# Kernel optimization log

Measured on AMD Instinct MI355X. Metric: run time of the kernel, lower is better.

## Reference

```python
import jax, jax.numpy as jnp
import numpy as np
import math

S, B, D, H = 2048, 4, 1024, 16
DH = D // H

def setup_inputs() -> dict:
    key = jax.random.key(0)
    ks = jax.random.split(key, 6)
    x = jax.random.normal(ks[0], (S, B, D), dtype=jnp.float32)
    # causal additive mask (finite large negative for numerical safety)
    i = jnp.arange(S)
    attn_mask = jnp.where(i[None, :] > i[:, None], jnp.float32(-1e9), jnp.float32(0.0))
    beta = jnp.zeros((H,), dtype=jnp.float32)  # per-head log-scale, init 0 -> exp=1
    xav = math.sqrt(6.0 / (D + D))  # xavier_uniform bound
    Wq = jax.random.uniform(ks[1], (D, D), minval=-xav, maxval=xav, dtype=jnp.float32)
    Wk = jax.random.uniform(ks[2], (D, D), minval=-xav, maxval=xav, dtype=jnp.float32)
    Wv = jax.random.uniform(ks[3], (D, D), minval=-xav, maxval=xav, dtype=jnp.float32)
    Wo = jax.random.uniform(ks[4], (D, D), minval=-xav, maxval=xav, dtype=jnp.float32)
    z = jnp.zeros((D,), dtype=jnp.float32)
    return {"x": x, "attn_mask": attn_mask, "beta": beta,
            "Wq": Wq, "bq": z, "Wk": Wk, "bk": z, "Wv": Wv, "bv": z, "Wo": Wo, "bo": z}

def reference(x, attn_mask, beta, Wq, bq, Wk, bk, Wv, bv, Wo, bo):
    s, b, d = x.shape
    h, dh = H, DH
    q = x @ Wq.T + bq  # (s, b, d)
    k = x @ Wk.T + bk
    v = x @ Wv.T + bv
    # attn_sink: append zero key/value token, pad mask with a zero column
    k = jnp.concatenate([k, jnp.zeros((1, b, d), k.dtype)], axis=0)  # (s+1, b, d)
    v = jnp.concatenate([v, jnp.zeros((1, b, d), v.dtype)], axis=0)
    mask = jnp.pad(attn_mask, ((0, 0), (0, 1)))  # (s, s+1)
    t = s + 1
    # split heads: (seq, b, h, dh) -> (b, h, seq, dh)
    qh = q.reshape(s, b, h, dh).transpose(1, 2, 0, 3)
    kh = k.reshape(t, b, h, dh).transpose(1, 2, 0, 3)
    vh = v.reshape(t, b, h, dh).transpose(1, 2, 0, 3)
    scale = (jnp.exp(beta) * math.sqrt(dh))[None, :, None, None]
    qh = qh / scale
    scores = jnp.einsum('bhsd,bhtd->bhst', qh, kh) + mask[None, None]
    w = jax.nn.softmax(scores, axis=-1)
    out = jnp.einsum('bhst,bhtd->bhsd', w, vh)  # (b, h, s, dh)
    out = out.transpose(2, 0, 1, 3).reshape(s, b, d)
    return out @ Wo.T + bo
```

## Files before the change

kernel.cpp:

```cpp
#include <hip/hip_runtime.h>
#include <hip/hip_bf16.h>
#include <math.h>

#define S_LEN   2048
#define BATCH   4
#define DMODEL  1024
#define NHEAD   16
#define DHEAD   64
#define MROWS   (S_LEN * BATCH)

typedef __bf16 bf16;
typedef __bf16 bf16x8 __attribute__((ext_vector_type(8)));
typedef __bf16 bf16x4 __attribute__((ext_vector_type(4)));
typedef short  short4_t __attribute__((ext_vector_type(4)));
typedef float  f32x4  __attribute__((ext_vector_type(4)));

#define LOG2E 1.4426950408889634f

#define AS1C(p) (const __attribute__((address_space(1))) void*)(p)
#define AS3(p)  (__attribute__((address_space(3))) void*)(p)


__global__ __launch_bounds__(256) void cast_bf16(const float* __restrict__ in,
                                                 bf16* __restrict__ out, int n8) {
    int i = blockIdx.x * 256 + threadIdx.x;
    if (i >= n8) return;
    const float4* p = (const float4*)in;
    float4 a = p[i * 2], b = p[i * 2 + 1];
    bf16x8 o;
    o[0] = (bf16)a.x; o[1] = (bf16)a.y; o[2] = (bf16)a.z; o[3] = (bf16)a.w;
    o[4] = (bf16)b.x; o[5] = (bf16)b.y; o[6] = (bf16)b.z; o[7] = (bf16)b.w;
    *(bf16x8*)(out + (size_t)i * 8) = o;
}

__global__ __launch_bounds__(256) void cast3_bf16(const float* __restrict__ w0,
                                                  const float* __restrict__ w1,
                                                  const float* __restrict__ w2,
                                                  bf16* __restrict__ out) {
    const int seg = blockIdx.y;
    const float* in = (seg == 0) ? w0 : (seg == 1) ? w1 : w2;
    int i = blockIdx.x * 256 + threadIdx.x;
    const float4* p = (const float4*)in;
    float4 a = p[i * 2], b = p[i * 2 + 1];
    bf16x8 o;
    o[0] = (bf16)a.x; o[1] = (bf16)a.y; o[2] = (bf16)a.z; o[3] = (bf16)a.w;
    o[4] = (bf16)b.x; o[5] = (bf16)b.y; o[6] = (bf16)b.z; o[7] = (bf16)b.w;
    *(bf16x8*)(out + (size_t)seg * DMODEL * DMODEL + (size_t)i * 8) = o;
}

#define GEMM_CORE(A_, W_, KDIM_)                                                        \
    constexpr int BK = 32;                                                              \
    __shared__ __align__(16) bf16 sA[128 * BK];                                         \
    __shared__ __align__(16) bf16 sB[128 * BK];                                         \
    const int t    = threadIdx.x;                                                       \
    const int lane = t & 63;                                                            \
    const int wave = t >> 6;                                                            \
    const int bm = blockIdx.y * 128;                                                    \
    const int wm = (wave & 1) * 64;                                                     \
    const int wn = (wave >> 1) * 64;                                                    \
    const int lq = lane & 15;                                                           \
    const int lg = lane >> 4;                                                           \
    const int grow = wave * 32 + (lane >> 2);                                           \
    const int gcol = (lane & 3) * 8;                                                    \
    const bf16* Ap = A_ + (size_t)(bm + grow) * KDIM_ + gcol;                           \
    const bf16* Wp = W_ + (size_t)(bn + grow) * KDIM_ + gcol;                           \
    bf16* la0 = &sA[(wave * 32) * BK];                                                  \
    bf16* lb0 = &sB[(wave * 32) * BK];                                                  \
    f32x4 acc[4][4] = {};                                                               \
    for (int k0 = 0; k0 < KDIM_; k0 += BK) {                                            \
        __syncthreads();                                                                \
        __builtin_amdgcn_global_load_lds(AS1C(Ap + k0),                      AS3(la0),           16, 0, 0); \
        __builtin_amdgcn_global_load_lds(AS1C(Ap + (size_t)16 * KDIM_ + k0), AS3(la0 + 16 * BK), 16, 0, 0); \
        __builtin_amdgcn_global_load_lds(AS1C(Wp + k0),                      AS3(lb0),           16, 0, 0); \
        __builtin_amdgcn_global_load_lds(AS1C(Wp + (size_t)16 * KDIM_ + k0), AS3(lb0 + 16 * BK), 16, 0, 0); \
        __syncthreads();                                                                \
        const int koff = lg * 8;                                                        \
        bf16x8 af[4], bfr[4];                                                           \
        _Pragma("unroll")                                                               \
        for (int mt = 0; mt < 4; mt++)                                                  \
            af[mt] = *(const bf16x8*)&sA[(wm + mt * 16 + lq) * BK + koff];              \
        _Pragma("unroll")                                                               \
        for (int nt = 0; nt < 4; nt++)                                                  \
            bfr[nt] = *(const bf16x8*)&sB[(wn + nt * 16 + lq) * BK + koff];             \
        _Pragma("unroll")                                                               \
        for (int mt = 0; mt < 4; mt++)                                                  \
            _Pragma("unroll")                                                           \
            for (int nt = 0; nt < 4; nt++)                                              \
                acc[mt][nt] = __builtin_amdgcn_mfma_f32_16x16x32_bf16(                  \
                    af[mt], bfr[nt], acc[mt][nt], 0, 0, 0);                             \
    }                                                                                   \
    const int cr = lg * 4;                                                              \
    const int cc = lq;

__global__ __launch_bounds__(256) void qkv_gemm(const bf16* __restrict__ A,
                                                const bf16* __restrict__ W,
                                                const float* __restrict__ bq,
                                                const float* __restrict__ bk,
                                                const float* __restrict__ bv,
                                                const float* __restrict__ beta,
                                                bf16* __restrict__ Qo,
                                                bf16* __restrict__ Kp,
                                                bf16* __restrict__ Vp) {
    const int bn = blockIdx.x * 128;
    GEMM_CORE(A, W, DMODEL)

    const int seg = blockIdx.x >> 3;
    const int bnl = (blockIdx.x & 7) * 128;
    const float* bias = (seg == 0) ? bq : (seg == 1) ? bk : bv;

    if (seg == 0) {
#pragma unroll
        for (int nt = 0; nt < 4; nt++) {
            const int col = bnl + wn + nt * 16 + cc;
            const float bvv = bias[col];
            const float sc = LOG2E / (__expf(beta[col >> 6]) * 8.0f);
#pragma unroll
            for (int mt = 0; mt < 4; mt++) {
                const int row = bm + wm + mt * 16 + cr;
#pragma unroll
                for (int r = 0; r < 4; r++) {
                    float v = (acc[mt][nt][r] + bvv) * sc;
                    Qo[(size_t)(row + r) * DMODEL + col] = (bf16)v;
                }
            }
        }
    } else {
        bf16* out = (seg == 1) ? Kp : Vp;
        const int h = (bnl + wn) >> 6;
#pragma unroll
        for (int mt = 0; mt < 4; mt++) {
            const int S0  = (bm + wm + mt * 16) >> 2;
            const int t16 = S0 >> 4;
            const int m4  = (S0 >> 2) & 3;
#pragma unroll
            for (int nt = 0; nt < 4; nt++) {
                const int col = bnl + wn + nt * 16 + cc;
                const float bvv = bias[col];
#pragma unroll
                for (int r = 0; r < 4; r++) {
                    float v = acc[mt][nt][r] + bvv;
                    size_t addr;
                    if (seg == 1) {
                        addr = ((size_t)((r * 16 + h) * 128 + t16)) * 1024
                             + (nt >> 1) * 512
                             + ((S0 & 15) + lg + 16 * ((nt & 1) * 2 + (lq >> 3))) * 8
                             + (lq & 7);
                    } else {
                        addr = ((size_t)((r * 16 + h) * 128 + t16)) * 1024
                             + nt * 256 + (lq + 16 * m4) * 4 + lg;
                    }
                    out[addr] = (bf16)v;
                }
            }
        }
    }
}

__global__ __launch_bounds__(256) void gemm_out(const bf16* __restrict__ A,
                                                const bf16* __restrict__ W,
                                                const float* __restrict__ bias,
                                                float* __restrict__ C) {
    const int bn = blockIdx.x * 128;
    GEMM_CORE(A, W, DMODEL)
#pragma unroll
    for (int nt = 0; nt < 4; nt++) {
        const int col = bn + wn + nt * 16 + cc;
        const float bvv = bias[col];
#pragma unroll
        for (int mt = 0; mt < 4; mt++) {
            const int row = bm + wm + mt * 16 + cr;
#pragma unroll
            for (int r = 0; r < 4; r++)
                C[(size_t)(row + r) * DMODEL + col] = acc[mt][nt][r] + bvv;
        }
    }
}

__global__ __launch_bounds__(256, 3) void attn_kernel(const bf16* __restrict__ Q,
                                                      const bf16* __restrict__ Kp,
                                                      const bf16* __restrict__ Vp,
                                                      bf16* __restrict__ O) {
    __shared__ __align__(16) float sO[64 * 65];
    __shared__ __align__(16) float sL[256];

    const int t    = threadIdx.x;
    const int lane = t & 63;
    const int wave = t >> 6;
    const int lq = lane & 15;
    const int lg = lane >> 4;

    const int bid = (int)blockIdx.x + 32 * ((int)blockIdx.y + 16 * (int)blockIdx.z);
    const int swz = (bid & 7) * 256 + (bid >> 3);
    const int qi  = 31 - (swz & 31);
    const int h   = (swz >> 5) & 15;
    const int b   = swz >> 9;
    const int qb  = qi * 64;

    bf16x8 qf[4][2];
#pragma unroll
    for (int nt = 0; nt < 4; nt++)
#pragma unroll
        for (int kc = 0; kc < 2; kc++)
            qf[nt][kc] = *(const bf16x8*)
                &Q[((size_t)(qb + nt * 16 + lq) * BATCH + b) * DMODEL + h * DHEAD + kc * 32 + lg * 8];

    f32x4 o_acc[4][4] = {};
    float l_lane[4] = {0.f, 0.f, 0.f, 0.f};

    const bf16* Kb = Kp + (size_t)(b * NHEAD + h) * 131072;
    const bf16* Vb = Vp + (size_t)(b * NHEAD + h) * 131072;

    bf16x8 kc0 = *(const bf16x8*)(Kb + (size_t)wave * 1024 + lane * 8);
    bf16x8 kc1 = *(const bf16x8*)(Kb + (size_t)wave * 1024 + 512 + lane * 8);
    bf16x4 vc0 = *(const bf16x4*)(Vb + (size_t)wave * 1024 +   0 + lane * 4);
    bf16x4 vc1 = *(const bf16x4*)(Vb + (size_t)wave * 1024 + 256 + lane * 4);
    bf16x4 vc2 = *(const bf16x4*)(Vb + (size_t)wave * 1024 + 512 + lane * 4);
    bf16x4 vc3 = *(const bf16x4*)(Vb + (size_t)wave * 1024 + 768 + lane * 4);

    for (int kt = 0; kt <= qi; kt++) {
        const int tn = ((kt < qi) ? (kt + 1) : 0) * 4 + wave;
        const bf16* Kn = Kb + (size_t)tn * 1024;
        const bf16* Vn = Vb + (size_t)tn * 1024;
        bf16x8 kn0 = *(const bf16x8*)(Kn + lane * 8);
        bf16x8 kn1 = *(const bf16x8*)(Kn + 512 + lane * 8);
        bf16x4 vn0 = *(const bf16x4*)(Vn +   0 + lane * 4);
        bf16x4 vn1 = *(const bf16x4*)(Vn + 256 + lane * 4);
        bf16x4 vn2 = *(const bf16x4*)(Vn + 512 + lane * 4);
        bf16x4 vn3 = *(const bf16x4*)(Vn + 768 + lane * 4);

        f32x4 st[4];
        __builtin_amdgcn_s_setprio(1);
#pragma unroll
        for (int nt = 0; nt < 4; nt++) {
            f32x4 a = {};
            a = __builtin_amdgcn_mfma_f32_16x16x32_bf16(kc0, qf[nt][0], a, 0, 0, 0);
            a = __builtin_amdgcn_mfma_f32_16x16x32_bf16(kc1, qf[nt][1], a, 0, 0, 0);
            st[nt] = a;
        }
        __builtin_amdgcn_s_setprio(0);

        if (kt == qi) {
#pragma unroll
            for (int nt = 0; nt < 4; nt++)
#pragma unroll
                for (int r = 0; r < 4; r++)
                    if (wave * 16 + lg * 4 + r > nt * 16 + lq) st[nt][r] = -1e30f;
        }

        short4_t pf[4];
#pragma unroll
        for (int nt = 0; nt < 4; nt++) {
            float p0 = __builtin_amdgcn_exp2f(st[nt][0]);
            float p1 = __builtin_amdgcn_exp2f(st[nt][1]);
            float p2 = __builtin_amdgcn_exp2f(st[nt][2]);
            float p3 = __builtin_amdgcn_exp2f(st[nt][3]);
            l_lane[nt] += (p0 + p1) + (p2 + p3);
            bf16x4 pv;
            pv[0] = (bf16)p0; pv[1] = (bf16)p1; pv[2] = (bf16)p2; pv[3] = (bf16)p3;
            pf[nt] = __builtin_bit_cast(short4_t, pv);
        }

        short4_t va0 = __builtin_bit_cast(short4_t, vc0);
        short4_t va1 = __builtin_bit_cast(short4_t, vc1);
        short4_t va2 = __builtin_bit_cast(short4_t, vc2);
        short4_t va3 = __builtin_bit_cast(short4_t, vc3);
        __builtin_amdgcn_s_setprio(1);
#pragma unroll
        for (int nt = 0; nt < 4; nt++) {
            o_acc[0][nt] = __builtin_amdgcn_mfma_f32_16x16x16bf16_1k(va0, pf[nt], o_acc[0][nt], 0, 0, 0);
            o_acc[1][nt] = __builtin_amdgcn_mfma_f32_16x16x16bf16_1k(va1, pf[nt], o_acc[1][nt], 0, 0, 0);
            o_acc[2][nt] = __builtin_amdgcn_mfma_f32_16x16x16bf16_1k(va2, pf[nt], o_acc[2][nt], 0, 0, 0);
            o_acc[3][nt] = __builtin_amdgcn_mfma_f32_16x16x16bf16_1k(va3, pf[nt], o_acc[3][nt], 0, 0, 0);
        }
        __builtin_amdgcn_s_setprio(0);

        kc0 = kn0; kc1 = kn1;
        vc0 = vn0; vc1 = vn1; vc2 = vn2; vc3 = vn3;
    }

#pragma unroll
    for (int nt = 0; nt < 4; nt++) {
        float v = l_lane[nt];
        v += __shfl_xor(v, 16);
        v += __shfl_xor(v, 32);
        if (lg == 0) sL[wave * 64 + nt * 16 + lq] = v;
    }

#pragma unroll
    for (int rd = 0; rd < 4; rd++) {
#pragma unroll
        for (int dtc = 0; dtc < 4; dtc++) {
            if (((wave + rd) & 3) == dtc) {
                if (rd == 0) {
#pragma unroll
                    for (int nt = 0; nt < 4; nt++)
#pragma unroll
                        for (int r = 0; r < 4; r++)
                            sO[(dtc * 16 + lg * 4 + r) * 65 + nt * 16 + lq] = o_acc[dtc][nt][r];
                } else {
#pragma unroll
                    for (int nt = 0; nt < 4; nt++)
#pragma unroll
                        for (int r = 0; r < 4; r++)
                            sO[(dtc * 16 + lg * 4 + r) * 65 + nt * 16 + lq] += o_acc[dtc][nt][r];
                }
            }
        }
        __syncthreads();
    }

    const int dt = wave;
    float rec[4];
#pragma unroll
    for (int nt = 0; nt < 4; nt++) {
        float lt = 1.0f + sL[nt * 16 + lq] + sL[64 + nt * 16 + lq]
                 + sL[128 + nt * 16 + lq] + sL[192 + nt * 16 + lq];
        rec[nt] = 1.0f / lt;
    }
#pragma unroll
    for (int nt = 0; nt < 4; nt++) {
        bf16x4 ov;
#pragma unroll
        for (int r = 0; r < 4; r++)
            ov[r] = (bf16)(sO[(dt * 16 + lg * 4 + r) * 65 + nt * 16 + lq] * rec[nt]);
        *(bf16x4*)&O[((size_t)(qb + nt * 16 + lq) * BATCH + b) * DMODEL + h * DHEAD + dt * 16 + lg * 4] = ov;
    }
}

extern "C" void kernel_launch(void* const* d_in, const int* in_sizes, int n_in,
                              void* d_out, int out_size, void* d_ws, size_t ws_size,
                              hipStream_t stream) {
    const float* x    = (const float*)d_in[0];
    const float* beta = (const float*)d_in[2];
    const float* Wq   = (const float*)d_in[3];
    const float* bq   = (const float*)d_in[4];
    const float* Wk   = (const float*)d_in[5];
    const float* bk   = (const float*)d_in[6];
    const float* Wv   = (const float*)d_in[7];
    const float* bv   = (const float*)d_in[8];
    const float* Wo   = (const float*)d_in[9];
    const float* bo   = (const float*)d_in[10];
    float* out = (float*)d_out;

    char* ws = (char*)d_ws;
    size_t off = 0;
    auto alloc = [&](size_t bytes) -> void* {
        void* p = ws + off;
        off += (bytes + 255) & ~(size_t)255;
        return p;
    };
    const size_t xbytes = (size_t)MROWS * DMODEL * sizeof(bf16);
    const size_t wbytes = (size_t)DMODEL * DMODEL * sizeof(bf16);
    bf16* xb   = (bf16*)alloc(xbytes);
    bf16* wqkv = (bf16*)alloc(3 * wbytes);
    bf16* wob  = (bf16*)alloc(wbytes);
    bf16* qws  = (bf16*)alloc(xbytes);
    bf16* kpb  = (bf16*)alloc(xbytes);
    bf16* vpb  = (bf16*)alloc(xbytes);
    bf16* aob  = (bf16*)alloc(xbytes);

    const int nx8 = MROWS * DMODEL / 8;
    const int nw8 = DMODEL * DMODEL / 8;
    cast_bf16<<<(nx8 + 255) / 256, 256, 0, stream>>>(x, xb, nx8);
    cast_bf16<<<(nw8 + 255) / 256, 256, 0, stream>>>(Wo, wob, nw8);
    dim3 c3grid(nw8 / 256, 3);
    cast3_bf16<<<c3grid, 256, 0, stream>>>(Wq, Wk, Wv, wqkv);

    dim3 qgrid(3 * DMODEL / 128, MROWS / 128);
    qkv_gemm<<<qgrid, 256, 0, stream>>>(xb, wqkv, bq, bk, bv, beta, qws, kpb, vpb);

    dim3 agrid(S_LEN / 64, NHEAD, BATCH);
    attn_kernel<<<agrid, 256, 0, stream>>>(qws, kpb, vpb, aob);

    dim3 ogrid(DMODEL / 128, MROWS / 128);
    gemm_out<<<ogrid, 256, 0, stream>>>(aob, wob, bo, out);
}
```

Baseline: 286.1 us.

## Rewrite GEMM core with 256x128 tiles, triple-buffered LDS and swizzled layout

Replaces the single-buffered 128x128 GEMM core used by the QKV and output projections with a 512-thread, 256x128 tile core. It triple-buffers the LDS tiles using async global-to-LDS loads, waits with a partial vmcnt and one barrier per K step, XOR-swizzles LDS chunks to avoid bank conflicts, and raises MFMA priority with setprio. The goal is to overlap global loads with MFMA work and halve the syncs, at the cost of more LDS per block, fewer blocks in the grid and rewritten epilogue index maths.

Measured after the change: 289.8 us. Within noise of the previous version (+1.3%).

```diff
diff --git a/kernel.cpp b/kernel.cpp
--- a/kernel.cpp
+++ b/kernel.cpp
@@ -48,61 +48,87 @@
     *(bf16x8*)(out + (size_t)seg * DMODEL * DMODEL + (size_t)i * 8) = o;
 }
 
-#define GEMM_CORE(A_, W_, KDIM_)                                                        \
+#define GEMM_CORE8(A_, W_, KDIM_)                                                       \
     constexpr int BK = 32;                                                              \
-    __shared__ __align__(16) bf16 sA[128 * BK];                                         \
-    __shared__ __align__(16) bf16 sB[128 * BK];                                         \
+    constexpr int NT_ = (KDIM_) / BK;                                                   \
+    __shared__ __align__(16) bf16 sA[3][256 * BK];                                      \
+    __shared__ __align__(16) bf16 sB[3][128 * BK];                                      \
     const int t    = threadIdx.x;                                                       \
     const int lane = t & 63;                                                            \
     const int wave = t >> 6;                                                            \
-    const int bm = blockIdx.y * 128;                                                    \
-    const int wm = (wave & 1) * 64;                                                     \
-    const int wn = (wave >> 1) * 64;                                                    \
-    const int lq = lane & 15;                                                           \
-    const int lg = lane >> 4;                                                           \
-    const int grow = wave * 32 + (lane >> 2);                                           \
-    const int gcol = (lane & 3) * 8;                                                    \
-    const bf16* Ap = A_ + (size_t)(bm + grow) * KDIM_ + gcol;                           \
-    const bf16* Wp = W_ + (size_t)(bn + grow) * KDIM_ + gcol;                           \
-    bf16* la0 = &sA[(wave * 32) * BK];                                                  \
-    bf16* lb0 = &sB[(wave * 32) * BK];                                                  \
-    f32x4 acc[4][4] = {};                                                               \
-    for (int k0 = 0; k0 < KDIM_; k0 += BK) {                                            \
-        __syncthreads();                                                                \
-        __builtin_amdgcn_global_load_lds(AS1C(Ap + k0),                      AS3(la0),           16, 0, 0); \
-        __builtin_amdgcn_global_load_lds(AS1C(Ap + (size_t)16 * KDIM_ + k0), AS3(la0 + 16 * BK), 16, 0, 0); \
-        __builtin_amdgcn_global_load_lds(AS1C(Wp + k0),                      AS3(lb0),           16, 0, 0); \
-        __builtin_amdgcn_global_load_lds(AS1C(Wp + (size_t)16 * KDIM_ + k0), AS3(lb0 + 16 * BK), 16, 0, 0); \
-        __syncthreads();                                                                \
-        const int koff = lg * 8;                                                        \
-        bf16x8 af[4], bfr[4];                                                           \
+    const int wr   = wave >> 2;                                                         \
+    const int wc   = wave & 3;                                                          \
+    const int lq   = lane & 15;                                                         \
+    const int lg   = lane >> 4;                                                         \
+    const int bm   = blockIdx.y * 256;                                                  \
+            \
+    const int schunk = (lane & 3) ^ ((lane >> 3) & 3);                                  \
+    const bf16* ApS  = A_ + (size_t)(bm + wave * 32 + (lane >> 2)) * (KDIM_) + schunk * 8; \
+    const bf16* ApS2 = ApS + (size_t)16 * (KDIM_);                                      \
+    const bf16* WpS  = W_ + (size_t)(bn + wave * 16 + (lane >> 2)) * (KDIM_) + schunk * 8; \
+         \
+    const int koff = (lg ^ ((lq >> 1) & 3)) * 8;                                        \
+    f32x4 acc[8][2] = {};                                                               \
+                                        \
+    __builtin_amdgcn_global_load_lds(AS1C(ApS),       AS3(&sA[0][wave*1024]),       16,0,0); \
+    __builtin_amdgcn_global_load_lds(AS1C(ApS2),      AS3(&sA[0][wave*1024 + 512]), 16,0,0); \
+    __builtin_amdgcn_global_load_lds(AS1C(WpS),       AS3(&sB[0][wave*512]),        16,0,0); \
+    __builtin_amdgcn_global_load_lds(AS1C(ApS  + BK), AS3(&sA[1][wave*1024]),       16,0,0); \
+    __builtin_amdgcn_global_load_lds(AS1C(ApS2 + BK), AS3(&sA[1][wave*1024 + 512]), 16,0,0); \
+    __builtin_amdgcn_global_load_lds(AS1C(WpS  + BK), AS3(&sB[1][wave*512]),        16,0,0); \
+    asm volatile("s_waitcnt vmcnt(3)\n\ts_barrier" ::: "memory");                       \
+    int bi = 0, si = 2, st = 2;                                                         \
+    for (int tt = 0; tt < NT_; ++tt) {                                                  \
+        {             \
+            const size_t ko = (size_t)st * BK;                                          \
+            __builtin_amdgcn_global_load_lds(AS1C(ApS  + ko), AS3(&sA[si][wave*1024]),       16,0,0); \
+            __builtin_amdgcn_global_load_lds(AS1C(ApS2 + ko), AS3(&sA[si][wave*1024 + 512]), 16,0,0); \
+            __builtin_amdgcn_global_load_lds(AS1C(WpS  + ko), AS3(&sB[si][wave*512]),        16,0,0); \
+        }                                                                               \
+        const bf16* At = sA[bi];                                                        \
+        const bf16* Bt = sB[bi];                                                        \
+        bf16x8 bf0 = *(const bf16x8*)&Bt[(wc*32 +      lq)*BK + koff];                  \
+        bf16x8 bf1 = *(const bf16x8*)&Bt[(wc*32 + 16 + lq)*BK + koff];                  \
+        bf16x8 af0[4];                                                                  \
         _Pragma("unroll")                                                               \
         for (int mt = 0; mt < 4; mt++)                                                  \
-            af[mt] = *(const bf16x8*)&sA[(wm + mt * 16 + lq) * BK + koff];              \
+            af0[mt] = *(const bf16x8*)&At[(wr*128 + mt*16 + lq)*BK + koff];             \
+        __builtin_amdgcn_s_setprio(1);                                                  \
         _Pragma("unroll")                                                               \
-        for (int nt = 0; nt < 4; nt++)                                                  \
-            bfr[nt] = *(const bf16x8*)&sB[(wn + nt * 16 + lq) * BK + koff];             \
+        for (int mt = 0; mt < 4; mt++) {                                                \
+            acc[mt][0] = __builtin_amdgcn_mfma_f32_16x16x32_bf16(af0[mt], bf0, acc[mt][0],0,0,0); \
+            acc[mt][1] = __builtin_amdgcn_mfma_f32_16x16x32_bf16(af0[mt], bf1, acc[mt][1],0,0,0); \
+        }                                                                               \
+        __builtin_amdgcn_s_setprio(0);                                                  \
+        bf16x8 af1[4];                                                                  \
         _Pragma("unroll")                                                               \
         for (int mt = 0; mt < 4; mt++)                                                  \
-            _Pragma("unroll")                                                           \
-            for (int nt = 0; nt < 4; nt++)                                              \
-                acc[mt][nt] = __builtin_amdgcn_mfma_f32_16x16x32_bf16(                  \
-                    af[mt], bfr[nt], acc[mt][nt], 0, 0, 0);                             \
-    }                                                                                   \
-    const int cr = lg * 4;                                                              \
-    const int cc = lq;
-
-__global__ __launch_bounds__(256) void qkv_gemm(const bf16* __restrict__ A,
-                                                const bf16* __restrict__ W,
-                                                const float* __restrict__ bq,
-                                                const float* __restrict__ bk,
-                                                const float* __restrict__ bv,
-                                                const float* __restrict__ beta,
-                                                bf16* __restrict__ Qo,
-                                                bf16* __restrict__ Kp,
-                                                bf16* __restrict__ Vp) {
+            af1[mt] = *(const bf16x8*)&At[(wr*128 + (mt+4)*16 + lq)*BK + koff];         \
+        __builtin_amdgcn_s_setprio(1);                                                  \
+        _Pragma("unroll")                                                               \
+        for (int mt = 0; mt < 4; mt++) {                                                \
+            acc[mt+4][0] = __builtin_amdgcn_mfma_f32_16x16x32_bf16(af1[mt], bf0, acc[mt+4][0],0,0,0); \
+            acc[mt+4][1] = __builtin_amdgcn_mfma_f32_16x16x32_bf16(af1[mt], bf1, acc[mt+4][1],0,0,0); \
+        }                                                                               \
+        __builtin_amdgcn_s_setprio(0);                                                  \
+           \
+        asm volatile("s_waitcnt vmcnt(3)\n\ts_barrier" ::: "memory");                   \
+        bi = (bi == 2) ? 0 : bi + 1;                                                    \
+        si = (si == 2) ? 0 : si + 1;                                                    \
+        st = (st == NT_ - 1) ? 0 : st + 1;                                              \
+    }
+
+__global__ __launch_bounds__(512, 4) void qkv_gemm(const bf16* __restrict__ A,
+                                                   const bf16* __restrict__ W,
+                                                   const float* __restrict__ bq,
+                                                   const float* __restrict__ bk,
+                                                   const float* __restrict__ bv,
+                                                   const float* __restrict__ beta,
+                                                   bf16* __restrict__ Qo,
+                                                   bf16* __restrict__ Kp,
+                                                   bf16* __restrict__ Vp) {
     const int bn = blockIdx.x * 128;
-    GEMM_CORE(A, W, DMODEL)
+    GEMM_CORE8(A, W, DMODEL)
 
     const int seg = blockIdx.x >> 3;
     const int bnl = (blockIdx.x & 7) * 128;
@@ -110,13 +136,13 @@
 
     if (seg == 0) {
 #pragma unroll
-        for (int nt = 0; nt < 4; nt++) {
-            const int col = bnl + wn + nt * 16 + cc;
+        for (int nt = 0; nt < 2; nt++) {
+            const int col = bnl + wc * 32 + nt * 16 + lq;
             const float bvv = bias[col];
             const float sc = LOG2E / (__expf(beta[col >> 6]) * 8.0f);
 #pragma unroll
-            for (int mt = 0; mt < 4; mt++) {
-                const int row = bm + wm + mt * 16 + cr;
+            for (int mt = 0; mt < 8; mt++) {
+                const int row = bm + wr * 128 + mt * 16 + lg * 4;
 #pragma unroll
                 for (int r = 0; r < 4; r++) {
                     float v = (acc[mt][nt][r] + bvv) * sc;
@@ -126,28 +152,31 @@
         }
     } else {
         bf16* out = (seg == 1) ? Kp : Vp;
-        const int h = (bnl + wn) >> 6;
-#pragma unroll
-        for (int mt = 0; mt < 4; mt++) {
-            const int S0  = (bm + wm + mt * 16) >> 2;
-            const int t16 = S0 >> 4;
-            const int m4  = (S0 >> 2) & 3;
-#pragma unroll
-            for (int nt = 0; nt < 4; nt++) {
-                const int col = bnl + wn + nt * 16 + cc;
+#pragma unroll
+        for (int mt = 0; mt < 8; mt++) {
+            const int F   = bm + wr * 128 + mt * 16;
+            const int S0X = F >> 2;
+            const int T   = S0X >> 4;
+            const int sl  = (S0X & 15) + lg;
+#pragma unroll
+            for (int nt = 0; nt < 2; nt++) {
+                const int col = bnl + wc * 32 + nt * 16 + lq;
+                const int h   = col >> 6;
+                const int dh  = col & 63;
                 const float bvv = bias[col];
 #pragma unroll
                 for (int r = 0; r < 4; r++) {
                     float v = acc[mt][nt][r] + bvv;
                     size_t addr;
                     if (seg == 1) {
-                        addr = ((size_t)((r * 16 + h) * 128 + t16)) * 1024
-                             + (nt >> 1) * 512
-                             + ((S0 & 15) + lg + 16 * ((nt & 1) * 2 + (lq >> 3))) * 8
-                             + (lq & 7);
+                        addr = ((size_t)((r * 16 + h) * 128 + T)) * 1024
+                             + (dh >> 5) * 512
+                             + (sl + 16 * ((dh >> 3) & 3)) * 8
+                             + (dh & 7);
                     } else {
-                        addr = ((size_t)((r * 16 + h) * 128 + t16)) * 1024
-                             + nt * 256 + (lq + 16 * m4) * 4 + lg;
+                        addr = ((size_t)((r * 16 + h) * 128 + T)) * 1024
+                             + (dh >> 4) * 256 + ((dh & 15) + 16 * (sl >> 2)) * 4
+                             + (sl & 3);
                     }
                     out[addr] = (bf16)v;
                 }
@@ -156,19 +185,19 @@
     }
 }
 
-__global__ __launch_bounds__(256) void gemm_out(const bf16* __restrict__ A,
-                                                const bf16* __restrict__ W,
-                                                const float* __restrict__ bias,
-                                                float* __restrict__ C) {
+__global__ __launch_bounds__(512, 2) void gemm_out(const bf16* __restrict__ A,
+                                                   const bf16* __restrict__ W,
+                                                   const float* __restrict__ bias,
+                                                   float* __restrict__ C) {
     const int bn = blockIdx.x * 128;
-    GEMM_CORE(A, W, DMODEL)
-#pragma unroll
-    for (int nt = 0; nt < 4; nt++) {
-        const int col = bn + wn + nt * 16 + cc;
+    GEMM_CORE8(A, W, DMODEL)
+#pragma unroll
+    for (int nt = 0; nt < 2; nt++) {
+        const int col = bn + wc * 32 + nt * 16 + lq;
         const float bvv = bias[col];
 #pragma unroll
-        for (int mt = 0; mt < 4; mt++) {
-            const int row = bm + wm + mt * 16 + cr;
+        for (int mt = 0; mt < 8; mt++) {
+            const int row = bm + wr * 128 + mt * 16 + lg * 4;
 #pragma unroll
             for (int r = 0; r < 4; r++)
                 C[(size_t)(row + r) * DMODEL + col] = acc[mt][nt][r] + bvv;
@@ -366,12 +395,12 @@
     dim3 c3grid(nw8 / 256, 3);
     cast3_bf16<<<c3grid, 256, 0, stream>>>(Wq, Wk, Wv, wqkv);
 
-    dim3 qgrid(3 * DMODEL / 128, MROWS / 128);
-    qkv_gemm<<<qgrid, 256, 0, stream>>>(xb, wqkv, bq, bk, bv, beta, qws, kpb, vpb);
+    dim3 qgrid(3 * DMODEL / 128, MROWS / 256);
+    qkv_gemm<<<qgrid, 512, 0, stream>>>(xb, wqkv, bq, bk, bv, beta, qws, kpb, vpb);
 
     dim3 agrid(S_LEN / 64, NHEAD, BATCH);
     attn_kernel<<<agrid, 256, 0, stream>>>(qws, kpb, vpb, aob);
 
-    dim3 ogrid(DMODEL / 128, MROWS / 128);
-    gemm_out<<<ogrid, 256, 0, stream>>>(aob, wob, bo, out);
-}
+    dim3 ogrid(DMODEL / 128, MROWS / 256);
+    gemm_out<<<ogrid, 512, 0, stream>>>(aob, wob, bo, out);
+}
```

## Triple-buffer GEMM LDS loads with swizzled layout and larger QKV tile

Applied to the files above, without the earlier changes.

Replaces the shared GEMM macro with two kernels that keep three LDS stages in flight using global_load_lds and vmcnt-based waits, so each k-step needs one barrier instead of two. LDS rows are XOR-swizzled to cut bank conflicts, s_setprio is raised around MFMA bursts, and the QKV GEMM tile grows to 256x128 per block to reuse more data. The larger tile and triple buffering raise register and LDS use and halve the QKV grid, which may lower occupancy. The prefetch index wraps at the end, so the last two iterations issue loads that are never consumed.

After: 286.9 us. Within noise of the previous version (+0.3%).

```diff
diff --git a/kernel.cpp b/kernel.cpp
--- a/kernel.cpp
+++ b/kernel.cpp
@@ -48,61 +48,85 @@
     *(bf16x8*)(out + (size_t)seg * DMODEL * DMODEL + (size_t)i * 8) = o;
 }
 
-#define GEMM_CORE(A_, W_, KDIM_)                                                        \
-    constexpr int BK = 32;                                                              \
-    __shared__ __align__(16) bf16 sA[128 * BK];                                         \
-    __shared__ __align__(16) bf16 sB[128 * BK];                                         \
-    const int t    = threadIdx.x;                                                       \
-    const int lane = t & 63;                                                            \
-    const int wave = t >> 6;                                                            \
-    const int bm = blockIdx.y * 128;                                                    \
-    const int wm = (wave & 1) * 64;                                                     \
-    const int wn = (wave >> 1) * 64;                                                    \
-    const int lq = lane & 15;                                                           \
-    const int lg = lane >> 4;                                                           \
-    const int grow = wave * 32 + (lane >> 2);                                           \
-    const int gcol = (lane & 3) * 8;                                                    \
-    const bf16* Ap = A_ + (size_t)(bm + grow) * KDIM_ + gcol;                           \
-    const bf16* Wp = W_ + (size_t)(bn + grow) * KDIM_ + gcol;                           \
-    bf16* la0 = &sA[(wave * 32) * BK];                                                  \
-    bf16* lb0 = &sB[(wave * 32) * BK];                                                  \
-    f32x4 acc[4][4] = {};                                                               \
-    for (int k0 = 0; k0 < KDIM_; k0 += BK) {                                            \
-        __syncthreads();                                                                \
-        __builtin_amdgcn_global_load_lds(AS1C(Ap + k0),                      AS3(la0),           16, 0, 0); \
-        __builtin_amdgcn_global_load_lds(AS1C(Ap + (size_t)16 * KDIM_ + k0), AS3(la0 + 16 * BK), 16, 0, 0); \
-        __builtin_amdgcn_global_load_lds(AS1C(Wp + k0),                      AS3(lb0),           16, 0, 0); \
-        __builtin_amdgcn_global_load_lds(AS1C(Wp + (size_t)16 * KDIM_ + k0), AS3(lb0 + 16 * BK), 16, 0, 0); \
-        __syncthreads();                                                                \
-        const int koff = lg * 8;                                                        \
-        bf16x8 af[4], bfr[4];                                                           \
-        _Pragma("unroll")                                                               \
-        for (int mt = 0; mt < 4; mt++)                                                  \
-            af[mt] = *(const bf16x8*)&sA[(wm + mt * 16 + lq) * BK + koff];              \
-        _Pragma("unroll")                                                               \
-        for (int nt = 0; nt < 4; nt++)                                                  \
-            bfr[nt] = *(const bf16x8*)&sB[(wn + nt * 16 + lq) * BK + koff];             \
-        _Pragma("unroll")                                                               \
-        for (int mt = 0; mt < 4; mt++)                                                  \
-            _Pragma("unroll")                                                           \
-            for (int nt = 0; nt < 4; nt++)                                              \
-                acc[mt][nt] = __builtin_amdgcn_mfma_f32_16x16x32_bf16(                  \
-                    af[mt], bfr[nt], acc[mt][nt], 0, 0, 0);                             \
-    }                                                                                   \
-    const int cr = lg * 4;                                                              \
-    const int cc = lq;
-
-__global__ __launch_bounds__(256) void qkv_gemm(const bf16* __restrict__ A,
-                                                const bf16* __restrict__ W,
-                                                const float* __restrict__ bq,
-                                                const float* __restrict__ bk,
-                                                const float* __restrict__ bv,
-                                                const float* __restrict__ beta,
-                                                bf16* __restrict__ Qo,
-                                                bf16* __restrict__ Kp,
-                                                bf16* __restrict__ Vp) {
-    const int bn = blockIdx.x * 128;
-    GEMM_CORE(A, W, DMODEL)
+__global__ __launch_bounds__(256, 2) void qkv_gemm(const bf16* __restrict__ A,
+                                                   const bf16* __restrict__ W,
+                                                   const float* __restrict__ bq,
+                                                   const float* __restrict__ bk,
+                                                   const float* __restrict__ bv,
+                                                   const float* __restrict__ beta,
+                                                   bf16* __restrict__ Qo,
+                                                   bf16* __restrict__ Kp,
+                                                   bf16* __restrict__ Vp) {
+    constexpr int BK = 32;
+    constexpr int NTILES = DMODEL / BK;
+    __shared__ __align__(16) bf16 sA[3][256 * BK];
+    __shared__ __align__(16) bf16 sB[3][128 * BK];
+
+    const int t    = threadIdx.x;
+    const int lane = t & 63;
+    const int wave = t >> 6;
+    const int wr   = wave >> 1;
+    const int wc   = wave & 1;
+    const int lq   = lane & 15;
+    const int lg   = lane >> 4;
+    const int bn   = blockIdx.x * 128;
+    const int bm   = blockIdx.y * 256;
+
+    const int schunk = (lane & 3) ^ ((lane >> 3) & 3);
+    const bf16* ApS = A + (size_t)(bm + wave * 64 + (lane >> 2)) * DMODEL + schunk * 8;
+    const bf16* WpS = W + (size_t)(bn + wave * 32 + (lane >> 2)) * DMODEL + schunk * 8;
+    const int koff = (lg ^ ((lq >> 1) & 3)) * 8;
+
+    f32x4 acc[8][4] = {};
+
+#define QSTAGE(si_, ko_)                                                                              \
+    __builtin_amdgcn_global_load_lds(AS1C(ApS + (ko_)),               AS3(&sA[si_][(wave*64 +  0)*BK]), 16,0,0); \
+    __builtin_amdgcn_global_load_lds(AS1C(ApS + 16*DMODEL + (ko_)),   AS3(&sA[si_][(wave*64 + 16)*BK]), 16,0,0); \
+    __builtin_amdgcn_global_load_lds(AS1C(ApS + 32*DMODEL + (ko_)),   AS3(&sA[si_][(wave*64 + 32)*BK]), 16,0,0); \
+    __builtin_amdgcn_global_load_lds(AS1C(ApS + 48*DMODEL + (ko_)),   AS3(&sA[si_][(wave*64 + 48)*BK]), 16,0,0); \
+    __builtin_amdgcn_global_load_lds(AS1C(WpS + (ko_)),               AS3(&sB[si_][(wave*32 +  0)*BK]), 16,0,0); \
+    __builtin_amdgcn_global_load_lds(AS1C(WpS + 16*DMODEL + (ko_)),   AS3(&sB[si_][(wave*32 + 16)*BK]), 16,0,0);
+
+    QSTAGE(0, 0)
+    QSTAGE(1, BK)
+    asm volatile("s_waitcnt vmcnt(6)\n\ts_barrier" ::: "memory");
+
+    int bi = 0, si = 2, st = 2;
+    for (int tt = 0; tt < NTILES; ++tt) {
+        QSTAGE(si, (size_t)st * BK)
+        const bf16* At = sA[bi];
+        const bf16* Bt = sB[bi];
+        bf16x8 bfr[4];
+#pragma unroll
+        for (int nt = 0; nt < 4; nt++)
+            bfr[nt] = *(const bf16x8*)&Bt[(wc * 64 + nt * 16 + lq) * BK + koff];
+        bf16x8 af[4];
+#pragma unroll
+        for (int mt = 0; mt < 4; mt++)
+            af[mt] = *(const bf16x8*)&At[(wr * 128 + mt * 16 + lq) * BK + koff];
+        __builtin_amdgcn_s_setprio(1);
+#pragma unroll
+        for (int mt = 0; mt < 4; mt++)
+#pragma unroll
+            for (int nt = 0; nt < 4; nt++)
+                acc[mt][nt] = __builtin_amdgcn_mfma_f32_16x16x32_bf16(af[mt], bfr[nt], acc[mt][nt], 0, 0, 0);
+        __builtin_amdgcn_s_setprio(0);
+#pragma unroll
+        for (int mt = 0; mt < 4; mt++)
+            af[mt] = *(const bf16x8*)&At[(wr * 128 + (mt + 4) * 16 + lq) * BK + koff];
+        __builtin_amdgcn_s_setprio(1);
+#pragma unroll
+        for (int mt = 0; mt < 4; mt++)
+#pragma unroll
+            for (int nt = 0; nt < 4; nt++)
+                acc[mt + 4][nt] = __builtin_amdgcn_mfma_f32_16x16x32_bf16(af[mt], bfr[nt], acc[mt + 4][nt], 0, 0, 0);
+        __builtin_amdgcn_s_setprio(0);
+        asm volatile("s_waitcnt vmcnt(6)\n\ts_barrier" ::: "memory");
+        bi = (bi == 2) ? 0 : bi + 1;
+        si = (si == 2) ? 0 : si + 1;
+        st = (st == NTILES - 1) ? 0 : st + 1;
+    }
+#undef QSTAGE
 
     const int seg = blockIdx.x >> 3;
     const int bnl = (blockIdx.x & 7) * 128;
@@ -111,12 +135,12 @@
     if (seg == 0) {
 #pragma unroll
         for (int nt = 0; nt < 4; nt++) {
-            const int col = bnl + wn + nt * 16 + cc;
+            const int col = bnl + wc * 64 + nt * 16 + lq;
             const float bvv = bias[col];
             const float sc = LOG2E / (__expf(beta[col >> 6]) * 8.0f);
 #pragma unroll
-            for (int mt = 0; mt < 4; mt++) {
-                const int row = bm + wm + mt * 16 + cr;
+            for (int mt = 0; mt < 8; mt++) {
+                const int row = bm + wr * 128 + mt * 16 + lg * 4;
 #pragma unroll
                 for (int r = 0; r < 4; r++) {
                     float v = (acc[mt][nt][r] + bvv) * sc;
@@ -126,28 +150,31 @@
         }
     } else {
         bf16* out = (seg == 1) ? Kp : Vp;
-        const int h = (bnl + wn) >> 6;
-#pragma unroll
-        for (int mt = 0; mt < 4; mt++) {
-            const int S0  = (bm + wm + mt * 16) >> 2;
-            const int t16 = S0 >> 4;
-            const int m4  = (S0 >> 2) & 3;
+#pragma unroll
+        for (int mt = 0; mt < 8; mt++) {
+            const int F   = bm + wr * 128 + mt * 16;
+            const int S0X = F >> 2;
+            const int T   = S0X >> 4;
+            const int sl  = (S0X & 15) + lg;
 #pragma unroll
             for (int nt = 0; nt < 4; nt++) {
-                const int col = bnl + wn + nt * 16 + cc;
+                const int col = bnl + wc * 64 + nt * 16 + lq;
+                const int h   = col >> 6;
+                const int dh  = col & 63;
                 const float bvv = bias[col];
 #pragma unroll
                 for (int r = 0; r < 4; r++) {
                     float v = acc[mt][nt][r] + bvv;
                     size_t addr;
                     if (seg == 1) {
-                        addr = ((size_t)((r * 16 + h) * 128 + t16)) * 1024
-                             + (nt >> 1) * 512
-                             + ((S0 & 15) + lg + 16 * ((nt & 1) * 2 + (lq >> 3))) * 8
-                             + (lq & 7);
+                        addr = ((size_t)((r * 16 + h) * 128 + T)) * 1024
+                             + (dh >> 5) * 512
+                             + (sl + 16 * ((dh >> 3) & 3)) * 8
+                             + (dh & 7);
                     } else {
-                        addr = ((size_t)((r * 16 + h) * 128 + t16)) * 1024
-                             + nt * 256 + (lq + 16 * m4) * 4 + lg;
+                        addr = ((size_t)((r * 16 + h) * 128 + T)) * 1024
+                             + (dh >> 4) * 256 + ((dh & 15) + 16 * (sl >> 2)) * 4
+                             + (sl & 3);
                     }
                     out[addr] = (bf16)v;
                 }
@@ -156,19 +183,75 @@
     }
 }
 
-__global__ __launch_bounds__(256) void gemm_out(const bf16* __restrict__ A,
-                                                const bf16* __restrict__ W,
-                                                const float* __restrict__ bias,
-                                                float* __restrict__ C) {
-    const int bn = blockIdx.x * 128;
-    GEMM_CORE(A, W, DMODEL)
+__global__ __launch_bounds__(256, 2) void gemm_out(const bf16* __restrict__ A,
+                                                   const bf16* __restrict__ W,
+                                                   const float* __restrict__ bias,
+                                                   float* __restrict__ C) {
+    constexpr int BK = 32;
+    constexpr int NTILES = DMODEL / BK;
+    __shared__ __align__(16) bf16 sA[3][128 * BK];
+    __shared__ __align__(16) bf16 sB[3][128 * BK];
+
+    const int t    = threadIdx.x;
+    const int lane = t & 63;
+    const int wave = t >> 6;
+    const int wr   = wave >> 1;
+    const int wc   = wave & 1;
+    const int lq   = lane & 15;
+    const int lg   = lane >> 4;
+    const int bn   = blockIdx.x * 128;
+    const int bm   = blockIdx.y * 128;
+
+    const int schunk = (lane & 3) ^ ((lane >> 3) & 3);
+    const bf16* ApS = A + (size_t)(bm + wave * 32 + (lane >> 2)) * DMODEL + schunk * 8;
+    const bf16* WpS = W + (size_t)(bn + wave * 32 + (lane >> 2)) * DMODEL + schunk * 8;
+    const int koff = (lg ^ ((lq >> 1) & 3)) * 8;
+
+    f32x4 acc[4][4] = {};
+
+#define OSTAGE(si_, ko_)                                                                              \
+    __builtin_amdgcn_global_load_lds(AS1C(ApS + (ko_)),               AS3(&sA[si_][(wave*32 +  0)*BK]), 16,0,0); \
+    __builtin_amdgcn_global_load_lds(AS1C(ApS + 16*DMODEL + (ko_)),   AS3(&sA[si_][(wave*32 + 16)*BK]), 16,0,0); \
+    __builtin_amdgcn_global_load_lds(AS1C(WpS + (ko_)),               AS3(&sB[si_][(wave*32 +  0)*BK]), 16,0,0); \
+    __builtin_amdgcn_global_load_lds(AS1C(WpS + 16*DMODEL + (ko_)),   AS3(&sB[si_][(wave*32 + 16)*BK]), 16,0,0);
+
+    OSTAGE(0, 0)
+    OSTAGE(1, BK)
+    asm volatile("s_waitcnt vmcnt(4)\n\ts_barrier" ::: "memory");
+
+    int bi = 0, si = 2, st = 2;
+    for (int tt = 0; tt < NTILES; ++tt) {
+        OSTAGE(si, (size_t)st * BK)
+        const bf16* At = sA[bi];
+        const bf16* Bt = sB[bi];
+        bf16x8 bfr[4], af[4];
+#pragma unroll
+        for (int nt = 0; nt < 4; nt++)
+            bfr[nt] = *(const bf16x8*)&Bt[(wc * 64 + nt * 16 + lq) * BK + koff];
+#pragma unroll
+        for (int mt = 0; mt < 4; mt++)
+            af[mt] = *(const bf16x8*)&At[(wr * 64 + mt * 16 + lq) * BK + koff];
+        __builtin_amdgcn_s_setprio(1);
+#pragma unroll
+        for (int mt = 0; mt < 4; mt++)
+#pragma unroll
+            for (int nt = 0; nt < 4; nt++)
+                acc[mt][nt] = __builtin_amdgcn_mfma_f32_16x16x32_bf16(af[mt], bfr[nt], acc[mt][nt], 0, 0, 0);
+        __builtin_amdgcn_s_setprio(0);
+        asm volatile("s_waitcnt vmcnt(4)\n\ts_barrier" ::: "memory");
+        bi = (bi == 2) ? 0 : bi + 1;
+        si = (si == 2) ? 0 : si + 1;
+        st = (st == NTILES - 1) ? 0 : st + 1;
+    }
+#undef OSTAGE
+
 #pragma unroll
     for (int nt = 0; nt < 4; nt++) {
-        const int col = bn + wn + nt * 16 + cc;
+        const int col = bn + wc * 64 + nt * 16 + lq;
         const float bvv = bias[col];
 #pragma unroll
         for (int mt = 0; mt < 4; mt++) {
-            const int row = bm + wm + mt * 16 + cr;
+            const int row = bm + wr * 64 + mt * 16 + lg * 4;
 #pragma unroll
             for (int r = 0; r < 4; r++)
                 C[(size_t)(row + r) * DMODEL + col] = acc[mt][nt][r] + bvv;
@@ -366,7 +449,7 @@
     dim3 c3grid(nw8 / 256, 3);
     cast3_bf16<<<c3grid, 256, 0, stream>>>(Wq, Wk, Wv, wqkv);
 
-    dim3 qgrid(3 * DMODEL / 128, MROWS / 128);
+    dim3 qgrid(3 * DMODEL / 128, MROWS / 256);
     qkv_gemm<<<qgrid, 256, 0, stream>>>(xb, wqkv, bq, bk, bv, beta, qws, kpb, vpb);
 
     dim3 agrid(S_LEN / 64, NHEAD, BATCH);
```
